# Kernel tuning notes

Hardware: AMD Instinct MI355X
Metric: run time of the kernel (lower is better)

Reference implementation:

```python
import jax, jax.numpy as jnp
import numpy as np

K_SIZE = 3
CH_IN = 256
NFILT = 256

def setup_inputs() -> dict:
    key = jax.random.key(0)
    k1, k2 = jax.random.split(key)
    x = jax.random.normal(k1, (32, 56, 56, CH_IN), dtype=jnp.float32)
    stdv = 1.0 / np.sqrt(K_SIZE * K_SIZE * CH_IN)
    w = jax.random.normal(k2, (K_SIZE, K_SIZE, CH_IN, NFILT), dtype=jnp.float32) * stdv
    pruning_mask = jnp.ones((K_SIZE * K_SIZE * CH_IN, NFILT), dtype=jnp.float32)
    return {"x": x, "w": w, "pruning_mask": pruning_mask}

def _magnitude_aware_weight(w):
    # scale = mean |w| over (kh, kw, cin), per output filter; stop-gradient
    scale = jax.lax.stop_gradient(jnp.mean(jnp.abs(w), axis=(0, 1, 2), keepdims=True))
    bw_no_grad = scale * jnp.sign(w)
    clipped = jnp.clip(w, -1.0, 1.0)
    # STE: forward = scale*sign(w), backward = d(clip(w,-1,1))
    return jax.lax.stop_gradient(bw_no_grad) - jax.lax.stop_gradient(clipped) + clipped

def reference(x, w, pruning_mask):
    kernel = _magnitude_aware_weight(w) * pruning_mask.reshape(K_SIZE, K_SIZE, CH_IN, NFILT)
    out = jax.lax.conv_general_dilated(
        x, kernel,
        window_strides=(1, 1),
        padding="SAME",
        dimension_numbers=("NHWC", "HWIO", "NHWC"),
    )
    return out
```

## Files before the change

kernel.cpp:

```cpp
#include <hip/hip_runtime.h>

typedef unsigned short u16;
typedef u16 u16x8 __attribute__((ext_vector_type(8)));
typedef __bf16 bf16x8 __attribute__((ext_vector_type(8)));
typedef float f32x4 __attribute__((ext_vector_type(4)));

#define NPIX 100352
#define KTOT 2304
#define IMG_PAD (58 * 58 * 256)

static __device__ __forceinline__ u16 f2bf(float f) {
  unsigned u = __float_as_uint(f);
  return (u16)((u + 0x7fffu + ((u >> 16) & 1u)) >> 16);
}

static __device__ __forceinline__ void gld_lds16(const u16* g, u16* l) {
  __builtin_amdgcn_global_load_lds(
      (const __attribute__((address_space(1))) void*)g,
      (__attribute__((address_space(3))) void*)l, 16, 0, 0);
}

static __device__ __forceinline__ int ka_of(int kt) {
  const int khw = kt >> 2;
  const int q = (khw * 11) >> 5;
  const int r = khw - q * 3;
  return (q * 58 + r - 59) * 256 + (kt & 3) * 64;
}

__global__ void scale_accum_k(const float* __restrict__ w, float* __restrict__ scale) {
  const int t = threadIdx.x;
  const float* p = w + (long)blockIdx.x * 64 * 256 + t;
  float acc = 0.f;
#pragma unroll
  for (int e = 0; e < 64; ++e) acc += fabsf(p[(long)e * 256]);
  atomicAdd(&scale[t], acc);
}

__global__ void pack_w_k(const float* __restrict__ w, const float* __restrict__ mask,
                         const float* __restrict__ ssum, u16* __restrict__ wp) {
  __shared__ u16 t[128][33];
  const int k0 = blockIdx.x * 32;
  const int f0 = blockIdx.y * 128;
  const int tid = threadIdx.x;
#pragma unroll
  for (int i = 0; i < 16; ++i) {
    int idx = tid + i * 256;
    int kk = idx >> 7;
    int ff = idx & 127;
    long g = (long)(k0 + kk) * 256 + f0 + ff;
    float wv = w[g];
    float mv = mask[g];
    float sc = ssum[f0 + ff] * (1.0f / 2304.0f);
    float sg = (wv > 0.f) ? 1.f : ((wv < 0.f) ? -1.f : 0.f);
    t[ff][kk] = f2bf(sc * sg * mv);
  }
  __syncthreads();
#pragma unroll
  for (int i = 0; i < 8; ++i) {
    int idx = tid + i * 256;
    int row = idx >> 4;
    int c = idx & 15;
    unsigned v = (unsigned)t[row][2 * c] | ((unsigned)t[row][2 * c + 1] << 16);
    *(unsigned*)(wp + (long)(f0 + row) * KTOT + k0 + 2 * c) = v;
  }
}

__global__ __launch_bounds__(256) void fill_xpad3_k(const float* __restrict__ x,
                                                    u16* __restrict__ xp) {
  const int img = blockIdx.y;
  const int ph = blockIdx.x;
  u16* rowp = xp + ((img * 58 + ph) * 58) * 256;
  const bool irow = (ph >= 1 && ph <= 56);
  const float* xrow = x + ((long)img * 3136 + (ph - 1) * 56) * 256;
  for (int i = threadIdx.x; i < 58 * 32; i += 256) {
    const int pw = i >> 5;
    const int c8 = (i & 31) * 8;
    u16x8 v = {0, 0, 0, 0, 0, 0, 0, 0};
    if (irow && pw >= 1 && pw <= 56) {
      const float* s = xrow + (pw - 1) * 256 + c8;
      float4 a = *(const float4*)s;
      float4 b = *(const float4*)(s + 4);
      v[0] = f2bf(a.x); v[1] = f2bf(a.y); v[2] = f2bf(a.z); v[3] = f2bf(a.w);
      v[4] = f2bf(b.x); v[5] = f2bf(b.y); v[6] = f2bf(b.z); v[7] = f2bf(b.w);
    }
    *(u16x8*)(rowp + pw * 256 + c8) = v;
  }
}

#define STAGE_A3(kt, h, buf) do { const int _ka = ka_of(kt); \
    gld_lds16(aptr[(h)*2]     + _ka, (buf) + ldso[(h)*2]); \
    gld_lds16(aptr[(h)*2 + 1] + _ka, (buf) + ldso[(h)*2 + 1]); } while (0)
#define STAGE_B3(kt, h, buf) do { const int _kb = (kt) * 64; \
    gld_lds16(bptr[(h)*2]     + _kb, (buf) + ldso[(h)*2]); \
    gld_lds16(bptr[(h)*2 + 1] + _kb, (buf) + ldso[(h)*2 + 1]); } while (0)
#define STAGE_AB3(kt, Aw, Bw) do { STAGE_A3(kt, 1, Aw); STAGE_B3(kt, 0, Bw); } while (0)

#define PHASE(pp, ABUF, BBUF, STAGE_STMT, WAIT_STMT) do {                         \
    if ((pp) == 0) {                                                              \
      _Pragma("unroll") for (int ni = 0; ni < 4; ++ni)                            \
        _Pragma("unroll") for (int ct = 0; ct < 2; ++ct)                          \
          bv[ni][ct] = *(const bf16x8*)((BBUF) + bB + pcq[ct] + ni * 1024);       \
    }                                                                             \
    bf16x8 av[2][2];                                                              \
    _Pragma("unroll") for (int f = 0; f < 2; ++f)                                 \
      _Pragma("unroll") for (int ct = 0; ct < 2; ++ct)                            \
        av[f][ct] = *(const bf16x8*)((ABUF) + aB + pcq[ct] + (pp) * 2048 + f * 1024); \
    STAGE_STMT;                                                                   \
    WAIT_STMT;                                                                    \
    __builtin_amdgcn_s_barrier();                                                 \
    asm volatile("" ::: "memory");                                                \
    __builtin_amdgcn_s_setprio(1);                                                \
    _Pragma("unroll") for (int ct = 0; ct < 2; ++ct)                              \
      _Pragma("unroll") for (int f = 0; f < 2; ++f)                               \
        _Pragma("unroll") for (int ni = 0; ni < 4; ++ni)                          \
          acc[(pp) * 2 + f][ni] = __builtin_amdgcn_mfma_f32_16x16x32_bf16(        \
              av[f][ct], bv[ni][ct], acc[(pp) * 2 + f][ni], 0, 0, 0);             \
    __builtin_amdgcn_s_setprio(0);                                                \
    asm volatile("" ::: "memory");                                                \
    __builtin_amdgcn_s_barrier();                                                 \
    asm volatile("" ::: "memory");                                                \
  } while (0)

#define VMC8 asm volatile("s_waitcnt vmcnt(8)" ::: "memory")
#define VMC0 asm volatile("s_waitcnt vmcnt(0)" ::: "memory")
#define NOSTMT do { } while (0)

__global__ __launch_bounds__(512, 2) void conv_gemm9_k(
    const u16* __restrict__ xpad, const u16* __restrict__ wp, float* __restrict__ out) {
  __shared__ u16 As[3][256 * 64];
  __shared__ u16 Bs[2][256 * 64];

  const int tid = threadIdx.x;
  const int lane = tid & 63;
  const int wid = tid >> 6;

  const int orig = blockIdx.x;
  const int swz = (orig & 7) * 49 + (orig >> 3);
  const int m0 = swz * 256;

  const int lsub = lane >> 3;
  const int lc = (lane & 7) ^ lsub;
  const u16* aptr[4];
  const u16* bptr[4];
  int ldso[4];
#pragma unroll
  for (int q = 0; q < 4; ++q) {
    const int o = (q >> 1) * 16 + (q & 1) * 8 + wid;
    const int row = o * 8 + lsub;
    const int m = m0 + row;
    const int img = m / 3136, pix = m % 3136;
    aptr[q] = xpad + (long)img * IMG_PAD + ((pix / 56 + 1) * 58 + (pix % 56) + 1) * 256 + lc * 8;
    bptr[q] = wp + (long)row * KTOT + lc * 8;
    ldso[q] = o * 512;
  }

  const int lm = lane & 15, kq = lane >> 4;
  const int wm = wid >> 2, wn = wid & 3;
  int pcq[2];
  pcq[0] = (kq ^ (lm & 7)) * 8;
  pcq[1] = ((4 + kq) ^ (lm & 7)) * 8;
  const int aB = (wm * 128 + lm) * 64;
  const int bB = (wn * 64 + lm) * 64;

  f32x4 acc[8][4] = {};
  bf16x8 bv[4][2];

  STAGE_A3(0, 0, As[0]); STAGE_A3(0, 1, As[0]);
  STAGE_B3(0, 0, Bs[0]); STAGE_B3(0, 1, Bs[0]);
  STAGE_A3(1, 0, As[1]); STAGE_A3(1, 1, As[1]);
  STAGE_B3(1, 0, Bs[1]); STAGE_B3(1, 1, Bs[1]);
  VMC8;
  __builtin_amdgcn_s_barrier();
  asm volatile("" ::: "memory");

  for (int J6 = 0; J6 < 5; ++J6) {
    const int kt0 = J6 * 6;
#pragma unroll
    for (int u = 0; u < 6; ++u) {
      const int kt = kt0 + u;
      u16* Ar = As[u % 3];
      u16* Br = Bs[u & 1];
      u16* Aw = As[(u + 2) % 3];
      u16* Bw = Bs[u & 1];
      PHASE(0, Ar, Br, STAGE_A3(kt + 2, 0, Aw), NOSTMT);
      PHASE(1, Ar, Br, STAGE_AB3(kt + 2, Aw, Bw), NOSTMT);
      PHASE(2, Ar, Br, STAGE_B3(kt + 2, 1, Bw), NOSTMT);
      PHASE(3, Ar, Br, NOSTMT, VMC8);
    }
  }

#pragma unroll
  for (int u = 0; u < 6; ++u) {
    const int kt = 30 + u;
    u16* Ar = As[u % 3];
    u16* Br = Bs[u & 1];
    u16* Aw = As[(u + 2) % 3];
    u16* Bw = Bs[u & 1];
    if (u < 4) {
      PHASE(0, Ar, Br, STAGE_A3(kt + 2, 0, Aw), NOSTMT);
      PHASE(1, Ar, Br, STAGE_AB3(kt + 2, Aw, Bw), NOSTMT);
      PHASE(2, Ar, Br, STAGE_B3(kt + 2, 1, Bw), NOSTMT);
      PHASE(3, Ar, Br, NOSTMT, VMC8);
    } else if (u == 4) {
      PHASE(0, Ar, Br, NOSTMT, NOSTMT);
      PHASE(1, Ar, Br, NOSTMT, NOSTMT);
      PHASE(2, Ar, Br, NOSTMT, NOSTMT);
      PHASE(3, Ar, Br, NOSTMT, VMC0);
    } else {
      PHASE(0, Ar, Br, NOSTMT, NOSTMT);
      PHASE(1, Ar, Br, NOSTMT, NOSTMT);
      PHASE(2, Ar, Br, NOSTMT, NOSTMT);
      PHASE(3, Ar, Br, NOSTMT, NOSTMT);
    }
  }

  float* op = out + (long)(m0 + wm * 128 + kq * 4) * 256 + wn * 64 + lm;
#pragma unroll
  for (int mi = 0; mi < 8; ++mi) {
#pragma unroll
    for (int ni = 0; ni < 4; ++ni) {
      float* p = op + (long)mi * 16 * 256 + ni * 16;
      f32x4 v = acc[mi][ni];
      p[0] = v[0];
      p[256] = v[1];
      p[512] = v[2];
      p[768] = v[3];
    }
  }
}

__global__ __launch_bounds__(256) void conv_gemm_fb_k(
    const float* __restrict__ x, const u16* __restrict__ wp, float* __restrict__ out) {
  __shared__ u16 As[128 * 40];
  __shared__ u16 Bs[128 * 40];
  const int tid = threadIdx.x;
  const int m0 = blockIdx.x * 128;
  const int n0 = blockIdx.y * 128;
  const int cc = tid & 3;
  const int r0 = tid >> 2;
  const int gm0 = m0 + r0;
  const int gm1 = gm0 + 64;
  const int pix0 = gm0 % 3136, oh0 = pix0 / 56, ow0 = pix0 % 56;
  const int pix1 = gm1 % 3136, oh1 = pix1 / 56, ow1 = pix1 % 56;
  const int lane = tid & 63;
  const int wv = tid >> 6;
  const int wm = wv & 1, wn = wv >> 1;
  const int lm = lane & 15, kq = lane >> 4;
  const int aoff = (wm * 64 + lm) * 40 + kq * 8;
  const int boff = (wn * 64 + lm) * 40 + kq * 8;
  u16* as0 = As + r0 * 40 + cc * 8;
  u16* as1 = As + (r0 + 64) * 40 + cc * 8;
  u16* bs0 = Bs + r0 * 40 + cc * 8;
  u16* bs1 = Bs + (r0 + 64) * 40 + cc * 8;
  const u16* wr0 = wp + (long)(n0 + r0) * KTOT + cc * 8;
  const u16* wr1 = wr0 + (long)64 * KTOT;
  f32x4 acc[4][4] = {};
  for (int khw = 0; khw < 9; ++khw) {
    const int dh = khw / 3 - 1;
    const int dw = khw % 3 - 1;
    const bool v0 = ((unsigned)(oh0 + dh) < 56u) && ((unsigned)(ow0 + dw) < 56u);
    const bool v1 = ((unsigned)(oh1 + dh) < 56u) && ((unsigned)(ow1 + dw) < 56u);
    const long p0 = ((long)gm0 + dh * 56 + dw) * 256 + cc * 8;
    const long p1 = ((long)gm1 + dh * 56 + dw) * 256 + cc * 8;
    const u16* wk0 = wr0 + khw * 256;
    const u16* wk1 = wr1 + khw * 256;
    for (int ct = 0; ct < 8; ++ct) {
      const int ci0 = ct * 32;
      u16x8 a0 = {0,0,0,0,0,0,0,0}, a1 = {0,0,0,0,0,0,0,0};
      float4 l0 = make_float4(0,0,0,0), h0 = make_float4(0,0,0,0);
      float4 l1 = make_float4(0,0,0,0), h1 = make_float4(0,0,0,0);
      if (v0) { l0 = *(const float4*)(x + p0 + ci0); h0 = *(const float4*)(x + p0 + ci0 + 4); }
      if (v1) { l1 = *(const float4*)(x + p1 + ci0); h1 = *(const float4*)(x + p1 + ci0 + 4); }
      a0[0]=f2bf(l0.x); a0[1]=f2bf(l0.y); a0[2]=f2bf(l0.z); a0[3]=f2bf(l0.w);
      a0[4]=f2bf(h0.x); a0[5]=f2bf(h0.y); a0[6]=f2bf(h0.z); a0[7]=f2bf(h0.w);
      a1[0]=f2bf(l1.x); a1[1]=f2bf(l1.y); a1[2]=f2bf(l1.z); a1[3]=f2bf(l1.w);
      a1[4]=f2bf(h1.x); a1[5]=f2bf(h1.y); a1[6]=f2bf(h1.z); a1[7]=f2bf(h1.w);
      u16x8 b0 = *(const u16x8*)(wk0 + ci0);
      u16x8 b1 = *(const u16x8*)(wk1 + ci0);
      __syncthreads();
      *(u16x8*)as0 = a0; *(u16x8*)as1 = a1;
      *(u16x8*)bs0 = b0; *(u16x8*)bs1 = b1;
      __syncthreads();
      bf16x8 av[4], bvv[4];
#pragma unroll
      for (int i = 0; i < 4; ++i) av[i] = *(const bf16x8*)(As + aoff + i * 640);
#pragma unroll
      for (int i = 0; i < 4; ++i) bvv[i] = *(const bf16x8*)(Bs + boff + i * 640);
#pragma unroll
      for (int mi = 0; mi < 4; ++mi)
#pragma unroll
        for (int ni = 0; ni < 4; ++ni)
          acc[mi][ni] = __builtin_amdgcn_mfma_f32_16x16x32_bf16(av[mi], bvv[ni], acc[mi][ni], 0, 0, 0);
    }
  }
  float* op = out + (long)(m0 + wm * 64 + kq * 4) * 256 + n0 + wn * 64 + lm;
#pragma unroll
  for (int mi = 0; mi < 4; ++mi)
#pragma unroll
    for (int ni = 0; ni < 4; ++ni) {
      float* p = op + (long)mi * 16 * 256 + ni * 16;
      f32x4 v = acc[mi][ni];
      p[0] = v[0]; p[256] = v[1]; p[512] = v[2]; p[768] = v[3];
    }
}

extern "C" void kernel_launch(void* const* d_in, const int* in_sizes, int n_in,
                              void* d_out, int out_size, void* d_ws, size_t ws_size,
                              hipStream_t stream) {
  const float* x = (const float*)d_in[0];
  const float* w = (const float*)d_in[1];
  const float* mask = (const float*)d_in[2];
  float* out = (float*)d_out;

  float* scale = (float*)d_ws;
  u16* wp = (u16*)((char*)d_ws + 1088);
  u16* xpad = (u16*)((char*)d_ws + 1088 + 1179648);
  const size_t xpad_bytes = (size_t)32 * IMG_PAD * 2;
  const size_t need = 1088 + 1179648 + xpad_bytes;

  (void)hipMemsetAsync(d_ws, 0, 1088, stream);
  scale_accum_k<<<36, 256, 0, stream>>>(w, scale);
  pack_w_k<<<dim3(72, 2), 256, 0, stream>>>(w, mask, scale, wp);
  if (ws_size >= need) {
    fill_xpad3_k<<<dim3(58, 32), 256, 0, stream>>>(x, xpad);
    conv_gemm9_k<<<392, 512, 0, stream>>>(xpad, wp, out);
  } else {
    conv_gemm_fb_k<<<dim3(784, 2), 256, 0, stream>>>(x, wp, out);
  }
}
```

Measured before the change: 344.6 us.

## Double-buffer LDS register reads and reshape GEMM pipeline to two-stage ping-pong

```diff
diff --git a/kernel.cpp b/kernel.cpp
--- a/kernel.cpp
+++ b/kernel.cpp
@@ -87,48 +87,59 @@
   }
 }
 
-#define STAGE_A3(kt, h, buf) do { const int _ka = ka_of(kt); \
+#define STAGE_A8(kt, h, buf) do { const int _ka = ka_of(kt); \
     gld_lds16(aptr[(h)*2]     + _ka, (buf) + ldso[(h)*2]); \
     gld_lds16(aptr[(h)*2 + 1] + _ka, (buf) + ldso[(h)*2 + 1]); } while (0)
-#define STAGE_B3(kt, h, buf) do { const int _kb = (kt) * 64; \
+#define STAGE_B8(kt, h, buf) do { const int _kb = (kt) * 64; \
     gld_lds16(bptr[(h)*2]     + _kb, (buf) + ldso[(h)*2]); \
     gld_lds16(bptr[(h)*2 + 1] + _kb, (buf) + ldso[(h)*2 + 1]); } while (0)
-#define STAGE_AB3(kt, Aw, Bw) do { STAGE_A3(kt, 1, Aw); STAGE_B3(kt, 0, Bw); } while (0)
-
-#define PHASE(pp, ABUF, BBUF, STAGE_STMT, WAIT_STMT) do {                         \
-    if ((pp) == 0) {                                                              \
-      _Pragma("unroll") for (int ni = 0; ni < 4; ++ni)                            \
-        _Pragma("unroll") for (int ct = 0; ct < 2; ++ct)                          \
-          bv[ni][ct] = *(const bf16x8*)((BBUF) + bB + pcq[ct] + ni * 1024);       \
-    }                                                                             \
-    bf16x8 av[2][2];                                                              \
-    _Pragma("unroll") for (int f = 0; f < 2; ++f)                                 \
-      _Pragma("unroll") for (int ct = 0; ct < 2; ++ct)                            \
-        av[f][ct] = *(const bf16x8*)((ABUF) + aB + pcq[ct] + (pp) * 2048 + f * 1024); \
-    STAGE_STMT;                                                                   \
-    WAIT_STMT;                                                                    \
-    __builtin_amdgcn_s_barrier();                                                 \
-    asm volatile("" ::: "memory");                                                \
-    __builtin_amdgcn_s_setprio(1);                                                \
-    _Pragma("unroll") for (int ct = 0; ct < 2; ++ct)                              \
-      _Pragma("unroll") for (int f = 0; f < 2; ++f)                               \
-        _Pragma("unroll") for (int ni = 0; ni < 4; ++ni)                          \
-          acc[(pp) * 2 + f][ni] = __builtin_amdgcn_mfma_f32_16x16x32_bf16(        \
-              av[f][ct], bv[ni][ct], acc[(pp) * 2 + f][ni], 0, 0, 0);             \
-    __builtin_amdgcn_s_setprio(0);                                                \
-    asm volatile("" ::: "memory");                                                \
-    __builtin_amdgcn_s_barrier();                                                 \
-    asm volatile("" ::: "memory");                                                \
+
+#define RD_AV(set, buf, q) do { \
+    _Pragma("unroll") for (int f = 0; f < 2; ++f) \
+      _Pragma("unroll") for (int ct = 0; ct < 2; ++ct) \
+        av[set][f][ct] = *(const bf16x8*)((buf) + aB + pcq[ct] + (q) * 2048 + f * 1024); \
   } while (0)
 
-#define VMC8 asm volatile("s_waitcnt vmcnt(8)" ::: "memory")
+#define RD_BV(set, buf) do { \
+    _Pragma("unroll") for (int ni = 0; ni < 4; ++ni) \
+      _Pragma("unroll") for (int ct = 0; ct < 2; ++ct) \
+        bv[set][ni][ct] = *(const bf16x8*)((buf) + bB + pcq[ct] + ni * 1024); \
+  } while (0)
+
+#define MM(asid, bsid, pp) do { \
+    _Pragma("unroll") for (int ct = 0; ct < 2; ++ct) \
+      _Pragma("unroll") for (int f = 0; f < 2; ++f) \
+        _Pragma("unroll") for (int ni = 0; ni < 4; ++ni) \
+          acc[(pp)*2 + f][ni] = __builtin_amdgcn_mfma_f32_16x16x32_bf16( \
+              av[asid][f][ct], bv[bsid][ni][ct], acc[(pp)*2 + f][ni], 0, 0, 0); \
+  } while (0)
+
+#define PHASE2(pp, STAGE_STMT, WAIT_STMT, RDNEXT_STMT, POST_STMT, ASID, BSID) do { \
+    STAGE_STMT; \
+    WAIT_STMT; \
+    __builtin_amdgcn_s_barrier(); \
+    asm volatile("" ::: "memory"); \
+    RDNEXT_STMT; \
+    __builtin_amdgcn_sched_barrier(0); \
+    __builtin_amdgcn_s_setprio(1); \
+    MM(ASID, BSID, pp); \
+    __builtin_amdgcn_s_setprio(0); \
+    POST_STMT; \
+    asm volatile("" ::: "memory"); \
+    __builtin_amdgcn_s_barrier(); \
+    asm volatile("" ::: "memory"); \
+  } while (0)
+
+#define VMC4 asm volatile("s_waitcnt vmcnt(4)" ::: "memory")
 #define VMC0 asm volatile("s_waitcnt vmcnt(0)" ::: "memory")
 #define NOSTMT do { } while (0)
 
-__global__ __launch_bounds__(512, 2) void conv_gemm9_k(
+__global__ __launch_bounds__(512, 2) void conv_gemm10_k(
     const u16* __restrict__ xpad, const u16* __restrict__ wp, float* __restrict__ out) {
-  __shared__ u16 As[3][256 * 64];
-  __shared__ u16 Bs[2][256 * 64];
+  __shared__ u16 As0[256 * 64];
+  __shared__ u16 As1[256 * 64];
+  __shared__ u16 Bs0[256 * 64];
+  __shared__ u16 Bs1[256 * 64];
 
   const int tid = threadIdx.x;
   const int lane = tid & 63;
@@ -163,56 +174,37 @@
   const int bB = (wn * 64 + lm) * 64;
 
   f32x4 acc[8][4] = {};
-  bf16x8 bv[4][2];
-
-  STAGE_A3(0, 0, As[0]); STAGE_A3(0, 1, As[0]);
-  STAGE_B3(0, 0, Bs[0]); STAGE_B3(0, 1, Bs[0]);
-  STAGE_A3(1, 0, As[1]); STAGE_A3(1, 1, As[1]);
-  STAGE_B3(1, 0, Bs[1]); STAGE_B3(1, 1, Bs[1]);
-  VMC8;
+  bf16x8 av[2][2][2];
+  bf16x8 bv[2][4][2];
+
+  STAGE_B8(0, 0, Bs0); STAGE_B8(0, 1, Bs0);
+  STAGE_A8(0, 0, As0); STAGE_A8(0, 1, As0);
+  STAGE_B8(1, 0, Bs1); STAGE_B8(1, 1, Bs1);
+  VMC4;
   __builtin_amdgcn_s_barrier();
   asm volatile("" ::: "memory");
-
-  for (int J6 = 0; J6 < 5; ++J6) {
-    const int kt0 = J6 * 6;
-#pragma unroll
-    for (int u = 0; u < 6; ++u) {
-      const int kt = kt0 + u;
-      u16* Ar = As[u % 3];
-      u16* Br = Bs[u & 1];
-      u16* Aw = As[(u + 2) % 3];
-      u16* Bw = Bs[u & 1];
-      PHASE(0, Ar, Br, STAGE_A3(kt + 2, 0, Aw), NOSTMT);
-      PHASE(1, Ar, Br, STAGE_AB3(kt + 2, Aw, Bw), NOSTMT);
-      PHASE(2, Ar, Br, STAGE_B3(kt + 2, 1, Bw), NOSTMT);
-      PHASE(3, Ar, Br, NOSTMT, VMC8);
-    }
-  }
-
-#pragma unroll
-  for (int u = 0; u < 6; ++u) {
-    const int kt = 30 + u;
-    u16* Ar = As[u % 3];
-    u16* Br = Bs[u & 1];
-    u16* Aw = As[(u + 2) % 3];
-    u16* Bw = Bs[u & 1];
-    if (u < 4) {
-      PHASE(0, Ar, Br, STAGE_A3(kt + 2, 0, Aw), NOSTMT);
-      PHASE(1, Ar, Br, STAGE_AB3(kt + 2, Aw, Bw), NOSTMT);
-      PHASE(2, Ar, Br, STAGE_B3(kt + 2, 1, Bw), NOSTMT);
-      PHASE(3, Ar, Br, NOSTMT, VMC8);
-    } else if (u == 4) {
-      PHASE(0, Ar, Br, NOSTMT, NOSTMT);
-      PHASE(1, Ar, Br, NOSTMT, NOSTMT);
-      PHASE(2, Ar, Br, NOSTMT, NOSTMT);
-      PHASE(3, Ar, Br, NOSTMT, VMC0);
-    } else {
-      PHASE(0, Ar, Br, NOSTMT, NOSTMT);
-      PHASE(1, Ar, Br, NOSTMT, NOSTMT);
-      PHASE(2, Ar, Br, NOSTMT, NOSTMT);
-      PHASE(3, Ar, Br, NOSTMT, NOSTMT);
-    }
-  }
+  RD_AV(0, As0, 0);
+  RD_BV(0, Bs0);
+
+  for (int J = 0; J < 17; ++J) {
+    PHASE2(0, STAGE_A8(2 * J + 1, 0, As1), NOSTMT, RD_AV(1, As0, 1), NOSTMT, 0, 0);
+    PHASE2(1, STAGE_A8(2 * J + 1, 1, As1), NOSTMT, RD_AV(0, As0, 2), NOSTMT, 1, 0);
+    PHASE2(2, STAGE_B8(2 * J + 2, 0, Bs0), NOSTMT, RD_AV(1, As0, 3), NOSTMT, 0, 0);
+    PHASE2(3, STAGE_B8(2 * J + 2, 1, Bs0), VMC4,   RD_AV(0, As1, 0), RD_BV(1, Bs1), 1, 0);
+    PHASE2(0, STAGE_A8(2 * J + 2, 0, As0), NOSTMT, RD_AV(1, As1, 1), NOSTMT, 0, 1);
+    PHASE2(1, STAGE_A8(2 * J + 2, 1, As0), NOSTMT, RD_AV(0, As1, 2), NOSTMT, 1, 1);
+    PHASE2(2, STAGE_B8(2 * J + 3, 0, Bs1), NOSTMT, RD_AV(1, As1, 3), NOSTMT, 0, 1);
+    PHASE2(3, STAGE_B8(2 * J + 3, 1, Bs1), VMC4,   RD_AV(0, As0, 0), RD_BV(0, Bs0), 1, 1);
+  }
+
+  PHASE2(0, STAGE_A8(35, 0, As1), NOSTMT, RD_AV(1, As0, 1), NOSTMT, 0, 0);
+  PHASE2(1, STAGE_A8(35, 1, As1), NOSTMT, RD_AV(0, As0, 2), NOSTMT, 1, 0);
+  PHASE2(2, NOSTMT,               NOSTMT, RD_AV(1, As0, 3), NOSTMT, 0, 0);
+  PHASE2(3, NOSTMT,               VMC0,   RD_AV(0, As1, 0), RD_BV(1, Bs1), 1, 0);
+  PHASE2(0, NOSTMT,               NOSTMT, RD_AV(1, As1, 1), NOSTMT, 0, 1);
+  PHASE2(1, NOSTMT,               NOSTMT, RD_AV(0, As1, 2), NOSTMT, 1, 1);
+  PHASE2(2, NOSTMT,               NOSTMT, RD_AV(1, As1, 3), NOSTMT, 0, 1);
+  PHASE2(3, NOSTMT,               NOSTMT, NOSTMT,           NOSTMT, 1, 1);
 
   float* op = out + (long)(m0 + wm * 128 + kq * 4) * 256 + wn * 64 + lm;
 #pragma unroll
@@ -281,16 +273,16 @@
       *(u16x8*)as0 = a0; *(u16x8*)as1 = a1;
       *(u16x8*)bs0 = b0; *(u16x8*)bs1 = b1;
       __syncthreads();
-      bf16x8 av[4], bvv[4];
-#pragma unroll
-      for (int i = 0; i < 4; ++i) av[i] = *(const bf16x8*)(As + aoff + i * 640);
+      bf16x8 avv[4], bvv[4];
+#pragma unroll
+      for (int i = 0; i < 4; ++i) avv[i] = *(const bf16x8*)(As + aoff + i * 640);
 #pragma unroll
       for (int i = 0; i < 4; ++i) bvv[i] = *(const bf16x8*)(Bs + boff + i * 640);
 #pragma unroll
       for (int mi = 0; mi < 4; ++mi)
 #pragma unroll
         for (int ni = 0; ni < 4; ++ni)
-          acc[mi][ni] = __builtin_amdgcn_mfma_f32_16x16x32_bf16(av[mi], bvv[ni], acc[mi][ni], 0, 0, 0);
+          acc[mi][ni] = __builtin_amdgcn_mfma_f32_16x16x32_bf16(avv[mi], bvv[ni], acc[mi][ni], 0, 0, 0);
     }
   }
   float* op = out + (long)(m0 + wm * 64 + kq * 4) * 256 + n0 + wn * 64 + lm;
@@ -323,7 +315,7 @@
   pack_w_k<<<dim3(72, 2), 256, 0, stream>>>(w, mask, scale, wp);
   if (ws_size >= need) {
     fill_xpad3_k<<<dim3(58, 32), 256, 0, stream>>>(x, xpad);
-    conv_gemm9_k<<<392, 512, 0, stream>>>(xpad, wp, out);
+    conv_gemm10_k<<<392, 512, 0, stream>>>(xpad, wp, out);
   } else {
     conv_gemm_fb_k<<<dim3(784, 2), 256, 0, stream>>>(x, wp, out);
   }
```

New measurement: 337.7 us. -2.0%, faster.
